# Performance work log

Hardware: AMD Instinct MI355X
Metric: run time of the kernel (lower is better)

## Reference

```python
import jax, jax.numpy as jnp
import numpy as np

NUM_HEADS = 16


def setup_inputs() -> dict:
    key = jax.random.key(0)
    k1, k2, k3 = jax.random.split(key, 3)
    B, N, C = 8, 1024, 1024
    x = jax.random.normal(k1, (B, N, C), dtype=jnp.float32)
    w_qkv = jax.random.normal(k2, (3 * C, C), dtype=jnp.float32) * (C ** -0.5)
    w_proj = jax.random.normal(k3, (C, C), dtype=jnp.float32) * (C ** -0.5)
    b_proj = jnp.zeros((C,), dtype=jnp.float32)
    return {"x": x, "w_qkv": w_qkv, "w_proj": w_proj, "b_proj": b_proj}


def reference(x, w_qkv, w_proj, b_proj):
    B, N, C = x.shape
    H = NUM_HEADS
    d = C // H
    scale = d ** -0.5
    # qkv projection: (B, N, 3C) -> (3, B, H, N, d)
    qkv = jnp.einsum('bnc,oc->bno', x, w_qkv)
    qkv = qkv.reshape(B, N, 3, H, d).transpose(2, 0, 3, 1, 4)
    q, k, v = qkv[0], qkv[1], qkv[2]
    # spatial attention
    attn = jnp.einsum('bhnd,bhmd->bhnm', q, k) * scale
    attn = jax.nn.softmax(attn, axis=-1)
    out = jnp.einsum('bhnm,bhmd->bhnd', attn, v)
    out = out.transpose(0, 2, 1, 3).reshape(B, N, C)
    # output projection
    return jnp.einsum('bnc,oc->bno', out, w_proj) + b_proj
```

## Files before the change

### kernel.cpp

```cpp
#include <hip/hip_runtime.h>
#include <hip/hip_bf16.h>

typedef unsigned short u16;
typedef unsigned int u32;
typedef __bf16 bf16x8 __attribute__((ext_vector_type(8)));
typedef float f32x4 __attribute__((ext_vector_type(4)));

__device__ __forceinline__ u16 f2b(float f) {
    __bf16 h = (__bf16)f;
    return __builtin_bit_cast(u16, h);
}
__device__ __forceinline__ u32 f2b2(float lo, float hi) {
    return (u32)f2b(lo) | ((u32)f2b(hi) << 16);
}
__device__ __forceinline__ f32x4 mfma16(bf16x8 a, bf16x8 b, f32x4 c) {
    return __builtin_amdgcn_mfma_f32_16x16x32_bf16(a, b, c, 0, 0, 0);
}
__device__ __forceinline__ void async16(const u16* gsrc, u16* ldst) {
    __builtin_amdgcn_global_load_lds(
        (const __attribute__((address_space(1))) void*)gsrc,
        (__attribute__((address_space(3))) void*)ldst, 16, 0, 0);
}

__global__ __launch_bounds__(256) void cvt_all(const float* __restrict__ x,
                                               const float* __restrict__ wq,
                                               const float* __restrict__ wp,
                                               u16* __restrict__ xb,
                                               u16* __restrict__ wqb,
                                               u16* __restrict__ wpb) {
    int i = (blockIdx.x * 256 + threadIdx.x) * 4;
    const float* src; u16* dst; int off; float scl;
    if (i < 8388608)       { src = x;  dst = xb;  off = i;            scl = 1.f; }
    else if (i < 9437184)  { src = wq; dst = wqb; off = i - 8388608;  scl = 0.18033688f; }
    else if (i < 11534336) { src = wq; dst = wqb; off = i - 8388608;  scl = 1.f; }
    else                   { src = wp; dst = wpb; off = i - 11534336; scl = 1.f; }
    float4 f = *(const float4*)(src + off);
    ushort4 o;
    o.x = f2b(f.x * scl); o.y = f2b(f.y * scl);
    o.z = f2b(f.z * scl); o.w = f2b(f.w * scl);
    *(ushort4*)(dst + off) = o;
}

template <bool F32OUT>
__device__ __forceinline__ void gemm_core(const u16* __restrict__ A,
                                          const u16* __restrict__ B,
                                          void* __restrict__ Cptr,
                                          const float* __restrict__ bias,
                                          int N, int K, int bm, int bn,
                                          u16* As, u16* Bs) {
    const int tid  = threadIdx.x;
    const int lane = tid & 63, wid = tid >> 6;
    const int quad = lane >> 4, l16 = lane & 15;
    const int wm = (wid >> 1) * 64, wn = (wid & 1) * 64;
    const int srow = tid >> 2;
    const int scol = (tid & 3) * 8;

    const u16* Abase = A + (size_t)(bm * 128) * K + scol;
    const u16* Bbase = B + (size_t)(bn * 128) * K + scol;

    f32x4 acc[4][4] = {};

    for (int k0 = 0; k0 < K; k0 += 32) {
        __syncthreads();
        async16(Abase + (size_t)srow * K + k0,        &As[wid * 512]);
        async16(Abase + (size_t)(64 + srow) * K + k0, &As[2048 + wid * 512]);
        async16(Bbase + (size_t)srow * K + k0,        &Bs[wid * 512]);
        async16(Bbase + (size_t)(64 + srow) * K + k0, &Bs[2048 + wid * 512]);
        __syncthreads();
        bf16x8 af[4], bfr[4];
#pragma unroll
        for (int mt = 0; mt < 4; mt++)
            af[mt] = *(const bf16x8*)&As[(wm + mt * 16 + l16) * 32 + quad * 8];
#pragma unroll
        for (int nt = 0; nt < 4; nt++)
            bfr[nt] = *(const bf16x8*)&Bs[(wn + nt * 16 + l16) * 32 + quad * 8];
#pragma unroll
        for (int mt = 0; mt < 4; mt++)
#pragma unroll
            for (int nt = 0; nt < 4; nt++)
                acc[mt][nt] = mfma16(af[mt], bfr[nt], acc[mt][nt]);
    }
#pragma unroll
    for (int mt = 0; mt < 4; mt++) {
#pragma unroll
        for (int nt = 0; nt < 4; nt++) {
            int row = bm * 128 + wm + mt * 16 + quad * 4;
            int col = bn * 128 + wn + nt * 16 + l16;
            float bv = F32OUT ? bias[col] : 0.f;
#pragma unroll
            for (int r = 0; r < 4; r++) {
                if (F32OUT)
                    ((float*)Cptr)[(size_t)(row + r) * N + col] = acc[mt][nt][r] + bv;
                else
                    ((u16*)Cptr)[(size_t)(row + r) * N + col] = f2b(acc[mt][nt][r]);
            }
        }
    }
}

__global__ __launch_bounds__(256) void gemm_qkvt(const u16* __restrict__ xb,
                                                 const u16* __restrict__ wqkvb,
                                                 u16* __restrict__ qkb,
                                                 u16* __restrict__ vTb) {
    __shared__ u16 As[128 * 32];
    __shared__ u16 Bs[128 * 32];
    int id = blockIdx.x;
    if (id < 1024) {
        gemm_core<false>(xb, wqkvb, qkb, nullptr, 2048, 1024, id >> 4, id & 15, As, Bs);
    } else {
        int t = id - 1024;
        gemm_core<false>(wqkvb + (size_t)2048 * 1024, xb, vTb, nullptr,
                         8192, 1024, t >> 6, t & 63, As, Bs);
    }
}

__global__ __launch_bounds__(256) void gemm_proj(const u16* __restrict__ A,
                                                 const u16* __restrict__ B,
                                                 void* __restrict__ C,
                                                 const float* __restrict__ bias) {
    __shared__ u16 As[128 * 32];
    __shared__ u16 Bs[128 * 32];
    gemm_core<true>(A, B, C, bias, 1024, 1024, blockIdx.y, blockIdx.x, As, Bs);
}

__global__ __launch_bounds__(256, 4) void attn_kernel(const u16* __restrict__ qk,
                                                      const u16* __restrict__ vT,
                                                      u16* __restrict__ outb) {
    __shared__ u16 Ks[2][64 * 64];
    __shared__ u16 Vt[2][64 * 64];
    __shared__ u16 Ps[4 * 16 * 64];
    const int tid = threadIdx.x, lane = tid & 63, wid = tid >> 6;
    const int quad = lane >> 4, l16 = lane & 15;
    const int qt = blockIdx.x;
    const int bh = blockIdx.y;
    const int b = bh >> 4, h = bh & 15;
    const size_t base = (size_t)b * 1024;
    const int hoff = h * 64;

    const int sr_ = lane >> 3;
    const int sc_ = ((lane & 7) ^ sr_) * 8;
    const int sw = l16 & 7;

    const u16* qptr = qk + (base + qt * 64 + wid * 16 + l16) * 2048 + hoff + quad * 8;
    bf16x8 bq0 = *(const bf16x8*)qptr;
    bf16x8 bq1 = *(const bf16x8*)(qptr + 32);

    auto stage = [&](int kt, int bs) {
#pragma unroll
        for (int j = 0; j < 2; ++j) {
            int rg = wid * 16 + j * 8;
            async16(qk + (base + kt * 64 + rg + sr_) * 2048 + 1024 + hoff + sc_,
                    &Ks[bs][rg * 64]);
            async16(vT + (size_t)(hoff + rg + sr_) * 8192 + base + kt * 64 + sc_,
                    &Vt[bs][rg * 64]);
        }
    };
    stage(0, 0);

    f32x4 Oacc[4] = {};
    f32x4 lacc = {};
    bf16x8 vone;
#pragma unroll
    for (int i = 0; i < 8; ++i) vone[i] = (__bf16)1.0f;
    u16* Pw = &Ps[wid * (16 * 64)];

    for (int t = 0; t < 16; ++t) {
        const int cur = t & 1;
        __builtin_amdgcn_s_barrier();
        __builtin_amdgcn_sched_barrier(0);
        if (t < 15) {
            stage(t + 1, cur ^ 1);
            asm volatile("s_waitcnt vmcnt(4)" ::: "memory");
        } else {
            asm volatile("s_waitcnt vmcnt(0)" ::: "memory");
        }
        __builtin_amdgcn_s_barrier();
        __builtin_amdgcn_sched_barrier(0);

        f32x4 sacc[4] = {};
#pragma unroll
        for (int nt = 0; nt < 4; nt++) {
            int row = nt * 16 + l16;
            bf16x8 ak0 = *(const bf16x8*)&Ks[cur][row * 64 + ((quad ^ sw) << 3)];
            bf16x8 ak1 = *(const bf16x8*)&Ks[cur][row * 64 + (((4 + quad) ^ sw) << 3)];
            sacc[nt] = mfma16(ak0, bq0, sacc[nt]);
            sacc[nt] = mfma16(ak1, bq1, sacc[nt]);
        }

#pragma unroll
        for (int nt = 0; nt < 4; nt++) {
            float p0 = exp2f(sacc[nt][0]);
            float p1 = exp2f(sacc[nt][1]);
            float p2 = exp2f(sacc[nt][2]);
            float p3 = exp2f(sacc[nt][3]);
            uint2 pk; pk.x = f2b2(p0, p1); pk.y = f2b2(p2, p3);
            *(uint2*)&Pw[l16 * 64 + (((nt * 2 + (quad >> 1)) ^ sw) << 3) + ((quad & 1) << 2)] = pk;
        }

        asm volatile("s_waitcnt lgkmcnt(0)" ::: "memory");
        __builtin_amdgcn_wave_barrier();
        __builtin_amdgcn_sched_barrier(0);

#pragma unroll
        for (int kc = 0; kc < 2; kc++) {
            bf16x8 ap = *(const bf16x8*)&Pw[l16 * 64 + (((kc * 4 + quad) ^ sw) << 3)];
            lacc = mfma16(ap, vone, lacc);
#pragma unroll
            for (int nv = 0; nv < 4; nv++) {
                int row = nv * 16 + l16;
                bf16x8 bv = *(const bf16x8*)&Vt[cur][row * 64 + (((kc * 4 + quad) ^ sw) << 3)];
                Oacc[nv] = mfma16(ap, bv, Oacc[nv]);
            }
        }
    }

    float inv[4];
#pragma unroll
    for (int r = 0; r < 4; r++) inv[r] = 1.f / lacc[r];

#pragma unroll
    for (int nv = 0; nv < 4; nv++)
#pragma unroll
        for (int r = 0; r < 4; r++) {
            int row = qt * 64 + wid * 16 + quad * 4 + r;
            int col = hoff + nv * 16 + l16;
            outb[(base + row) * 1024 + col] = f2b(Oacc[nv][r] * inv[r]);
        }
}

extern "C" void kernel_launch(void* const* d_in, const int* in_sizes, int n_in,
                              void* d_out, int out_size, void* d_ws, size_t ws_size,
                              hipStream_t stream) {
    const float* x      = (const float*)d_in[0];
    const float* w_qkv  = (const float*)d_in[1];
    const float* w_proj = (const float*)d_in[2];
    const float* b_proj = (const float*)d_in[3];

    char* ws = (char*)d_ws;
    u16* xb     = (u16*)(ws);
    u16* wqkvb  = (u16*)(ws + 16777216);
    u16* wprojb = (u16*)(ws + 23068672);
    u16* qkb    = (u16*)(ws + 25165824);
    u16* vTb    = (u16*)(ws + 58720256);
    u16* attnb  = (u16*)(ws + 75497472);

    cvt_all<<<12288, 256, 0, stream>>>(x, w_qkv, w_proj, xb, wqkvb, wprojb);
    gemm_qkvt<<<1536, 256, 0, stream>>>(xb, wqkvb, qkb, vTb);
    attn_kernel<<<dim3(16, 128), 256, 0, stream>>>(qkb, vTb, attnb);
    gemm_proj<<<dim3(8, 64), 256, 0, stream>>>(attnb, wprojb, d_out, b_proj);
}
```

Before: 247.6 us.

## Double-buffer GEMM LDS tiles, swizzle QKV block order, software-pipeline attention PV

The GEMM core now double-buffers its A/B LDS tiles, so the next k-slice is prefetched asynchronously while the current one feeds MFMA, replacing the two full syncthreads per iteration. The QKV GEMM remaps block IDs to interleave tiles for better L2 locality. The attention kernel splits K and V staging and defers the P·V MFMAs of the previous tile so they interleave with the current tile's exp computation, with an epilogue for the last tile. LDS use for the GEMMs doubles, which may lower occupancy, and the reordered waits add risk to correctness.

```diff
diff --git a/kernel.cpp b/kernel.cpp
--- a/kernel.cpp
+++ b/kernel.cpp
@@ -58,22 +58,41 @@
     const u16* Abase = A + (size_t)(bm * 128) * K + scol;
     const u16* Bbase = B + (size_t)(bn * 128) * K + scol;
 
+    auto stage = [&](int k0, int buf) {
+        u16* as = As + buf * 4096;
+        u16* bs = Bs + buf * 4096;
+        async16(Abase + (size_t)srow * K + k0,        &as[wid * 512]);
+        async16(Abase + (size_t)(64 + srow) * K + k0, &as[2048 + wid * 512]);
+        async16(Bbase + (size_t)srow * K + k0,        &bs[wid * 512]);
+        async16(Bbase + (size_t)(64 + srow) * K + k0, &bs[2048 + wid * 512]);
+    };
+
     f32x4 acc[4][4] = {};
-
-    for (int k0 = 0; k0 < K; k0 += 32) {
-        __syncthreads();
-        async16(Abase + (size_t)srow * K + k0,        &As[wid * 512]);
-        async16(Abase + (size_t)(64 + srow) * K + k0, &As[2048 + wid * 512]);
-        async16(Bbase + (size_t)srow * K + k0,        &Bs[wid * 512]);
-        async16(Bbase + (size_t)(64 + srow) * K + k0, &Bs[2048 + wid * 512]);
-        __syncthreads();
+    stage(0, 0);
+    const int NT = K >> 5;
+
+    for (int t = 0; t < NT; ++t) {
+        const int cur = t & 1;
+        __builtin_amdgcn_s_barrier();
+        __builtin_amdgcn_sched_barrier(0);
+        if (t + 1 < NT) {
+            stage((t + 1) << 5, cur ^ 1);
+            asm volatile("s_waitcnt vmcnt(4)" ::: "memory");
+        } else {
+            asm volatile("s_waitcnt vmcnt(0)" ::: "memory");
+        }
+        __builtin_amdgcn_s_barrier();
+        __builtin_amdgcn_sched_barrier(0);
+
+        const u16* as = As + cur * 4096;
+        const u16* bs = Bs + cur * 4096;
         bf16x8 af[4], bfr[4];
 #pragma unroll
         for (int mt = 0; mt < 4; mt++)
-            af[mt] = *(const bf16x8*)&As[(wm + mt * 16 + l16) * 32 + quad * 8];
+            af[mt] = *(const bf16x8*)&as[(wm + mt * 16 + l16) * 32 + quad * 8];
 #pragma unroll
         for (int nt = 0; nt < 4; nt++)
-            bfr[nt] = *(const bf16x8*)&Bs[(wn + nt * 16 + l16) * 32 + quad * 8];
+            bfr[nt] = *(const bf16x8*)&bs[(wn + nt * 16 + l16) * 32 + quad * 8];
 #pragma unroll
         for (int mt = 0; mt < 4; mt++)
 #pragma unroll
@@ -102,9 +121,9 @@
                                                  const u16* __restrict__ wqkvb,
                                                  u16* __restrict__ qkb,
                                                  u16* __restrict__ vTb) {
-    __shared__ u16 As[128 * 32];
-    __shared__ u16 Bs[128 * 32];
-    int id = blockIdx.x;
+    __shared__ u16 As[2 * 128 * 32];
+    __shared__ u16 Bs[2 * 128 * 32];
+    int id = (blockIdx.x & 7) * 192 + (blockIdx.x >> 3);
     if (id < 1024) {
         gemm_core<false>(xb, wqkvb, qkb, nullptr, 2048, 1024, id >> 4, id & 15, As, Bs);
     } else {
@@ -118,8 +137,8 @@
                                                  const u16* __restrict__ B,
                                                  void* __restrict__ C,
                                                  const float* __restrict__ bias) {
-    __shared__ u16 As[128 * 32];
-    __shared__ u16 Bs[128 * 32];
+    __shared__ u16 As[2 * 128 * 32];
+    __shared__ u16 Bs[2 * 128 * 32];
     gemm_core<true>(A, B, C, bias, 1024, 1024, blockIdx.y, blockIdx.x, As, Bs);
 }
 
@@ -145,17 +164,23 @@
     bf16x8 bq0 = *(const bf16x8*)qptr;
     bf16x8 bq1 = *(const bf16x8*)(qptr + 32);
 
-    auto stage = [&](int kt, int bs) {
+    auto stageK = [&](int kt, int bs) {
 #pragma unroll
         for (int j = 0; j < 2; ++j) {
             int rg = wid * 16 + j * 8;
             async16(qk + (base + kt * 64 + rg + sr_) * 2048 + 1024 + hoff + sc_,
                     &Ks[bs][rg * 64]);
+        }
+    };
+    auto stageV = [&](int kt, int bs) {
+#pragma unroll
+        for (int j = 0; j < 2; ++j) {
+            int rg = wid * 16 + j * 8;
             async16(vT + (size_t)(hoff + rg + sr_) * 8192 + base + kt * 64 + sc_,
                     &Vt[bs][rg * 64]);
         }
     };
-    stage(0, 0);
+    stageK(0, 0);
 
     f32x4 Oacc[4] = {};
     f32x4 lacc = {};
@@ -163,17 +188,16 @@
 #pragma unroll
     for (int i = 0; i < 8; ++i) vone[i] = (__bf16)1.0f;
     u16* Pw = &Ps[wid * (16 * 64)];
-
-    for (int t = 0; t < 16; ++t) {
-        const int cur = t & 1;
+    bf16x8 ap0, ap1;
+
+    for (int u = 0; u < 16; ++u) {
+        const int cur = u & 1;
         __builtin_amdgcn_s_barrier();
         __builtin_amdgcn_sched_barrier(0);
-        if (t < 15) {
-            stage(t + 1, cur ^ 1);
-            asm volatile("s_waitcnt vmcnt(4)" ::: "memory");
-        } else {
-            asm volatile("s_waitcnt vmcnt(0)" ::: "memory");
-        }
+        if (u < 15) stageK(u + 1, cur ^ 1);
+        stageV(u, cur);
+        if (u < 15) asm volatile("s_waitcnt vmcnt(4)" ::: "memory");
+        else        asm volatile("s_waitcnt vmcnt(2)" ::: "memory");
         __builtin_amdgcn_s_barrier();
         __builtin_amdgcn_sched_barrier(0);
 
@@ -187,8 +211,17 @@
             sacc[nt] = mfma16(ak1, bq1, sacc[nt]);
         }
 
-#pragma unroll
-        for (int nt = 0; nt < 4; nt++) {
+        if (u) {
+            lacc = mfma16(ap0, vone, lacc);
+#pragma unroll
+            for (int nv = 0; nv < 4; nv++) {
+                int row = nv * 16 + l16;
+                bf16x8 bv = *(const bf16x8*)&Vt[cur ^ 1][row * 64 + ((quad ^ sw) << 3)];
+                Oacc[nv] = mfma16(ap0, bv, Oacc[nv]);
+            }
+        }
+#pragma unroll
+        for (int nt = 0; nt < 2; nt++) {
             float p0 = exp2f(sacc[nt][0]);
             float p1 = exp2f(sacc[nt][1]);
             float p2 = exp2f(sacc[nt][2]);
@@ -196,22 +229,48 @@
             uint2 pk; pk.x = f2b2(p0, p1); pk.y = f2b2(p2, p3);
             *(uint2*)&Pw[l16 * 64 + (((nt * 2 + (quad >> 1)) ^ sw) << 3) + ((quad & 1) << 2)] = pk;
         }
+        if (u) {
+            lacc = mfma16(ap1, vone, lacc);
+#pragma unroll
+            for (int nv = 0; nv < 4; nv++) {
+                int row = nv * 16 + l16;
+                bf16x8 bv = *(const bf16x8*)&Vt[cur ^ 1][row * 64 + (((4 + quad) ^ sw) << 3)];
+                Oacc[nv] = mfma16(ap1, bv, Oacc[nv]);
+            }
+        }
+#pragma unroll
+        for (int nt = 2; nt < 4; nt++) {
+            float p0 = exp2f(sacc[nt][0]);
+            float p1 = exp2f(sacc[nt][1]);
+            float p2 = exp2f(sacc[nt][2]);
+            float p3 = exp2f(sacc[nt][3]);
+            uint2 pk; pk.x = f2b2(p0, p1); pk.y = f2b2(p2, p3);
+            *(uint2*)&Pw[l16 * 64 + (((nt * 2 + (quad >> 1)) ^ sw) << 3) + ((quad & 1) << 2)] = pk;
+        }
 
         asm volatile("s_waitcnt lgkmcnt(0)" ::: "memory");
         __builtin_amdgcn_wave_barrier();
         __builtin_amdgcn_sched_barrier(0);
-
-#pragma unroll
-        for (int kc = 0; kc < 2; kc++) {
-            bf16x8 ap = *(const bf16x8*)&Pw[l16 * 64 + (((kc * 4 + quad) ^ sw) << 3)];
-            lacc = mfma16(ap, vone, lacc);
-#pragma unroll
-            for (int nv = 0; nv < 4; nv++) {
-                int row = nv * 16 + l16;
-                bf16x8 bv = *(const bf16x8*)&Vt[cur][row * 64 + (((kc * 4 + quad) ^ sw) << 3)];
-                Oacc[nv] = mfma16(ap, bv, Oacc[nv]);
-            }
-        }
+        ap0 = *(const bf16x8*)&Pw[l16 * 64 + ((quad ^ sw) << 3)];
+        ap1 = *(const bf16x8*)&Pw[l16 * 64 + (((4 + quad) ^ sw) << 3)];
+    }
+
+    asm volatile("s_waitcnt vmcnt(0)" ::: "memory");
+    __builtin_amdgcn_s_barrier();
+    __builtin_amdgcn_sched_barrier(0);
+    lacc = mfma16(ap0, vone, lacc);
+#pragma unroll
+    for (int nv = 0; nv < 4; nv++) {
+        int row = nv * 16 + l16;
+        bf16x8 bv = *(const bf16x8*)&Vt[1][row * 64 + ((quad ^ sw) << 3)];
+        Oacc[nv] = mfma16(ap0, bv, Oacc[nv]);
+    }
+    lacc = mfma16(ap1, vone, lacc);
+#pragma unroll
+    for (int nv = 0; nv < 4; nv++) {
+        int row = nv * 16 + l16;
+        bf16x8 bv = *(const bf16x8*)&Vt[1][row * 64 + (((4 + quad) ^ sw) << 3)];
+        Oacc[nv] = mfma16(ap1, bv, Oacc[nv]);
     }
 
     float inv[4];
```

Measured after the change: 262.7 us. 6.1% more time.
